# Kernel optimization log

Measured on AMD Instinct MI355X. Metric: run time of the kernel, lower is better.

The kernel has to match this reference:

```python
import jax, jax.numpy as jnp
import numpy as np

N_NODES = 100000
N_EDGES = 1600000
IN_CH = 128
HID = 32
HEADS = 4
OUT_CH = 32
NEG_SLOPE = 0.2  # PyG GATConv default


def _gat_conv(x, src, dst, W, a_src, a_dst, bias, concat):
    """One GATConv layer (eval mode, self-loops already in src/dst).
    x: [N, F_in], W: [F_in, H*C], a_src/a_dst: [H, C], bias: [H*C] or [C].
    """
    N = x.shape[0]
    H, C = a_src.shape
    h = (x @ W).reshape(N, H, C)                      # [N, H, C]
    alpha_s = jnp.einsum('nhc,hc->nh', h, a_src)      # [N, H]
    alpha_d = jnp.einsum('nhc,hc->nh', h, a_dst)      # [N, H]
    logits = jax.nn.leaky_relu(alpha_s[src] + alpha_d[dst], NEG_SLOPE)  # [E, H]
    # segment softmax over incoming edges of each destination node
    m = jax.ops.segment_max(logits, dst, num_segments=N)   # [N, H]
    e = jnp.exp(logits - m[dst])                            # [E, H]
    denom = jax.ops.segment_sum(e, dst, num_segments=N)     # [N, H]
    alpha = e / denom[dst]                                   # [E, H]
    msg = h[src] * alpha[:, :, None]                         # [E, H, C]
    out = jax.ops.segment_sum(msg, dst, num_segments=N)     # [N, H, C]
    out = out.reshape(N, H * C) if concat else out.mean(axis=1)
    return out + bias


def setup_inputs() -> dict:
    key = jax.random.key(0)
    ks = jax.random.split(key, 12)
    x = jax.random.normal(ks[0], (N_NODES, IN_CH), dtype=jnp.float32)
    edge_index = jax.random.randint(ks[1], (2, N_EDGES), 0, N_NODES, dtype=jnp.int64)
    g = 0.1  # glorot-ish scale
    W1 = jax.random.normal(ks[2], (IN_CH, HEADS * HID), dtype=jnp.float32) * g
    a_src1 = jax.random.normal(ks[3], (HEADS, HID), dtype=jnp.float32) * g
    a_dst1 = jax.random.normal(ks[4], (HEADS, HID), dtype=jnp.float32) * g
    b1 = jnp.zeros((HEADS * HID,), dtype=jnp.float32)
    W2 = jax.random.normal(ks[5], (HEADS * HID, OUT_CH), dtype=jnp.float32) * g
    a_src2 = jax.random.normal(ks[6], (1, OUT_CH), dtype=jnp.float32) * g
    a_dst2 = jax.random.normal(ks[7], (1, OUT_CH), dtype=jnp.float32) * g
    b2 = jnp.zeros((OUT_CH,), dtype=jnp.float32)
    return {"x": x, "edge_index": edge_index,
            "W1": W1, "a_src1": a_src1, "a_dst1": a_dst1, "b1": b1,
            "W2": W2, "a_src2": a_src2, "a_dst2": a_dst2, "b2": b2}


def reference(x, edge_index, W1, a_src1, a_dst1, b1, W2, a_src2, a_dst2, b2):
    N = x.shape[0]
    loops = jnp.arange(N, dtype=edge_index.dtype)
    src = jnp.concatenate([edge_index[0], loops])  # add self-loops (PyG default)
    dst = jnp.concatenate([edge_index[1], loops])
    h = _gat_conv(x, src, dst, W1, a_src1, a_dst1, b1, concat=True)   # [N, H*HID]
    h = jax.nn.elu(h)
    out = _gat_conv(h, src, dst, W2, a_src2, a_dst2, b2, concat=False)  # [N, OUT]
    return out
```

## Files before the change

### kernel.cpp

```cpp
#include <hip/hip_runtime.h>
#include <math.h>

#define N_NODES 100000
#define N_EDGES 1600000
#define E_TOT   1700000
#define NEG_SLOPE 0.2f
#define NBUCK 196
#define G1_BLOCKS 1563
#define SCAT_BLOCKS 831
#define PREP_BLOCKS 64

typedef unsigned short ushort_t;
typedef unsigned int uint_t;
typedef __attribute__((ext_vector_type(8))) short bf16x8;
typedef __attribute__((ext_vector_type(4))) float f32x4;

__device__ __forceinline__ float lrelu(float v) { return v > 0.f ? v : NEG_SLOPE * v; }
__device__ __forceinline__ float bf16lo(uint_t u) { return __uint_as_float(u << 16); }
__device__ __forceinline__ float bf16hi(uint_t u) { return __uint_as_float(u & 0xffff0000u); }
__device__ __forceinline__ ushort_t f2bf(float f) {
    uint_t u = __float_as_uint(f);
    u += 0x7fffu + ((u >> 16) & 1u);
    return (ushort_t)(u >> 16);
}

union BU { uint4 u; bf16x8 b; };

__global__ __launch_bounds__(256) void k_prep_hist(const float* __restrict__ W,
                                                   ushort_t* __restrict__ Wb,
                                                   const int* __restrict__ ei,
                                                   int* __restrict__ bucket_cnt)
{
    __shared__ int lbin[NBUCK];
    const int t = threadIdx.x;

    if (blockIdx.x < PREP_BLOCKS) {
        const int idx = blockIdx.x * 256 + t;
        const int j  = idx & 7;
        const int kq = (idx >> 3) & 3;
        const int n  = (idx >> 5) & 15;
        const int tc = (idx >> 9) & 7;
        const int kc = idx >> 12;
        Wb[idx] = f2bf(W[(kc * 32 + kq * 8 + j) * 128 + tc * 16 + n]);
        return;
    }

    const int e0 = (blockIdx.x - PREP_BLOCKS) * 2048 + t;
    for (int i = t; i < NBUCK; i += 256) lbin[i] = 0;
    __syncthreads();
#pragma unroll
    for (int i = 0; i < 8; ++i) {
        const int e = e0 + i * 256;
        if (e < E_TOT) {
            const int d = (e < N_EDGES) ? ei[N_EDGES + e] : (e - N_EDGES);
            atomicAdd(&lbin[d >> 9], 1);
        }
    }
    __syncthreads();
    for (int i = t; i < NBUCK; i += 256)
        if (lbin[i]) atomicAdd(&bucket_cnt[i], lbin[i]);
}

__global__ __launch_bounds__(256) void k_scanB(const int* __restrict__ bucket_cnt,
                                               int* __restrict__ bucket_base,
                                               int* __restrict__ bucket_cursor)
{
    __shared__ int s[256];
    const int t = threadIdx.x;
    const int v = (t < NBUCK) ? bucket_cnt[t] : 0;
    s[t] = v; __syncthreads();
    for (int off = 1; off < 256; off <<= 1) {
        int a = (t >= off) ? s[t - off] : 0;
        __syncthreads();
        s[t] += a;
        __syncthreads();
    }
    const int excl = s[t] - v;
    if (t < NBUCK) {
        bucket_base[t] = excl;
        bucket_cursor[t] = excl;
        if (t == NBUCK - 1) bucket_base[NBUCK] = excl + v;
    }
}

__global__ __launch_bounds__(256) void k_gemm1_scat(const float* __restrict__ x,
                                                    const ushort_t* __restrict__ Wb,
                                                    const float* __restrict__ a_src,
                                                    const float* __restrict__ a_dst,
                                                    ushort_t* __restrict__ hb,
                                                    float* __restrict__ as_,
                                                    float* __restrict__ ad_,
                                                    const int* __restrict__ ei,
                                                    int* __restrict__ bucket_cursor,
                                                    uint2* __restrict__ pairs)
{
    __shared__ int lcnt[NBUCK];
    __shared__ int lbase[NBUCK];
    const int t = threadIdx.x;

    if (blockIdx.x >= G1_BLOCKS) {
        const int e0 = (blockIdx.x - G1_BLOCKS) * 2048 + t;
        for (int i = t; i < NBUCK; i += 256) lcnt[i] = 0;
        __syncthreads();
        int s8[8], d8[8];
#pragma unroll
        for (int i = 0; i < 8; ++i) {
            const int e = e0 + i * 256;
            int s = -1, d = 0;
            if (e < E_TOT) {
                if (e < N_EDGES) { s = ei[e]; d = ei[N_EDGES + e]; }
                else { s = d = e - N_EDGES; }
                atomicAdd(&lcnt[d >> 9], 1);
            }
            s8[i] = s; d8[i] = d;
        }
        __syncthreads();
        for (int i = t; i < NBUCK; i += 256) {
            const int c = lcnt[i];
            lbase[i] = (c > 0) ? atomicAdd(&bucket_cursor[i], c) : 0;
        }
        __syncthreads();
        for (int i = t; i < NBUCK; i += 256) lcnt[i] = 0;
        __syncthreads();
#pragma unroll
        for (int i = 0; i < 8; ++i) {
            if (s8[i] >= 0) {
                const int b = d8[i] >> 9;
                const int pos = lbase[b] + atomicAdd(&lcnt[b], 1);
                pairs[pos] = make_uint2((uint_t)s8[i], (uint_t)d8[i]);
            }
        }
        return;
    }

    const int lane = t & 63;
    const int w = t >> 6;
    const int rbase = blockIdx.x * 64 + w * 16;
    const int li = lane & 15;
    const int g = lane >> 4;

    f32x4 acc[8];
#pragma unroll
    for (int tc = 0; tc < 8; ++tc) acc[tc] = (f32x4){0.f, 0.f, 0.f, 0.f};

    int arow = rbase + li;
    if (arow > N_NODES - 1) arow = N_NODES - 1;
    const float* xr = x + (size_t)arow * 128 + g * 8;

#pragma unroll
    for (int kc = 0; kc < 4; ++kc) {
        const float4 a0 = *(const float4*)(xr + kc * 32);
        const float4 a1 = *(const float4*)(xr + kc * 32 + 4);
        BU au;
        au.u.x = (uint_t)f2bf(a0.x) | ((uint_t)f2bf(a0.y) << 16);
        au.u.y = (uint_t)f2bf(a0.z) | ((uint_t)f2bf(a0.w) << 16);
        au.u.z = (uint_t)f2bf(a1.x) | ((uint_t)f2bf(a1.y) << 16);
        au.u.w = (uint_t)f2bf(a1.z) | ((uint_t)f2bf(a1.w) << 16);
        const bf16x8 af = au.b;
#pragma unroll
        for (int tc = 0; tc < 8; ++tc) {
            const bf16x8 bf = *(const bf16x8*)(Wb + (size_t)(kc * 8 + tc) * 512 + li * 32 + g * 8);
            acc[tc] = __builtin_amdgcn_mfma_f32_16x16x32_bf16(af, bf, acc[tc], 0, 0, 0);
        }
    }

#pragma unroll
    for (int r = 0; r < 4; ++r) {
        const int row = rbase + g * 4 + r;
        if (row < N_NODES) {
            ushort_t* hp = hb + (size_t)row * 128 + li;
#pragma unroll
            for (int tc = 0; tc < 8; ++tc) hp[tc * 16] = f2bf(acc[tc][r]);
        }
    }

    float asv[8], adv[8];
#pragma unroll
    for (int tc = 0; tc < 8; ++tc) {
        asv[tc] = a_src[tc * 16 + li];
        adv[tc] = a_dst[tc * 16 + li];
    }
#pragma unroll
    for (int h = 0; h < 4; ++h) {
#pragma unroll
        for (int r = 0; r < 4; ++r) {
            float ps = acc[2 * h][r] * asv[2 * h] + acc[2 * h + 1][r] * asv[2 * h + 1];
            float pd = acc[2 * h][r] * adv[2 * h] + acc[2 * h + 1][r] * adv[2 * h + 1];
            ps += __shfl_xor(ps, 1); pd += __shfl_xor(pd, 1);
            ps += __shfl_xor(ps, 2); pd += __shfl_xor(pd, 2);
            ps += __shfl_xor(ps, 4); pd += __shfl_xor(pd, 4);
            ps += __shfl_xor(ps, 8); pd += __shfl_xor(pd, 8);
            const int row = rbase + g * 4 + r;
            if (li == 0 && row < N_NODES) {
                as_[row * 4 + h] = ps;
                ad_[row * 4 + h] = pd;
            }
        }
    }
}

__global__ __launch_bounds__(512) void k_buildC(const uint2* __restrict__ pairs,
                                                const int* __restrict__ bucket_base,
                                                int* __restrict__ row_ptr,
                                                int* __restrict__ col_src)
{
    __shared__ int cnt[512];
    __shared__ int cur[512];
    const int b = blockIdx.x, t = threadIdx.x;
    const int bstart = bucket_base[b], bend = bucket_base[b + 1];
    const int node0 = b << 9;

    cnt[t] = 0;
    __syncthreads();
    for (int e = bstart + t; e < bend; e += 512)
        atomicAdd(&cnt[pairs[e].y - node0], 1);
    __syncthreads();

    const int v = cnt[t];
    cur[t] = v; __syncthreads();
    for (int off = 1; off < 512; off <<= 1) {
        int a = (t >= off) ? cur[t - off] : 0;
        __syncthreads();
        cur[t] += a;
        __syncthreads();
    }
    const int excl = bstart + cur[t] - v;
    const int node = node0 + t;
    if (node < N_NODES) row_ptr[node] = excl;
    if (b == 0 && t == 0) row_ptr[N_NODES] = E_TOT;
    cur[t] = excl;
    __syncthreads();

    for (int e = bstart + t; e < bend; e += 512) {
        const uint2 pr = pairs[e];
        const int pos = atomicAdd(&cur[pr.y - node0], 1);
        col_src[pos] = (int)pr.x;
    }
}

__global__ __launch_bounds__(64) void k_agg1(const ushort_t* __restrict__ hb,
                                             const float* __restrict__ as_,
                                             const float* __restrict__ ad_,
                                             const int* __restrict__ row_ptr,
                                             const int* __restrict__ col_src,
                                             const float* __restrict__ bias,
                                             ushort_t* __restrict__ x2b)
{
    __shared__ float sEx[256];
    __shared__ int sSrc[64];
    const int n = blockIdx.x;
    const int lane = threadIdx.x;
    const int start = row_ptr[n], end = row_ptr[n + 1];
    const float4 adv = *(const float4*)(ad_ + (size_t)n * 4);

    const int hsel = lane >> 4;
    const int c0 = lane * 2;
    float2 acc = make_float2(0.f, 0.f);
    float4 ds = make_float4(0.f, 0.f, 0.f, 0.f);
    for (int base = start; base < end; base += 64) {
        const int e = base + lane;
        const int cnt = min(64, end - base);
        float4 ex = make_float4(0.f, 0.f, 0.f, 0.f);
        int s = 0;
        if (e < end) {
            s = col_src[e];
            const float4 av = *(const float4*)(as_ + (size_t)s * 4);
            ex.x = __expf(lrelu(av.x + adv.x));
            ex.y = __expf(lrelu(av.y + adv.y));
            ex.z = __expf(lrelu(av.z + adv.z));
            ex.w = __expf(lrelu(av.w + adv.w));
            ds.x += ex.x; ds.y += ex.y; ds.z += ex.z; ds.w += ex.w;
        }
        __syncthreads();
        *(float4*)(sEx + lane * 4) = ex;
        sSrc[lane] = s;
        __syncthreads();
        for (int i = 0; i < cnt; ++i) {
            const float w = sEx[i * 4 + hsel];
            const uint_t hv = *(const uint_t*)(hb + (size_t)sSrc[i] * 128 + c0);
            acc.x = fmaf(w, bf16lo(hv), acc.x);
            acc.y = fmaf(w, bf16hi(hv), acc.y);
        }
    }
#pragma unroll
    for (int off = 32; off > 0; off >>= 1) {
        ds.x += __shfl_xor(ds.x, off);
        ds.y += __shfl_xor(ds.y, off);
        ds.z += __shfl_xor(ds.z, off);
        ds.w += __shfl_xor(ds.w, off);
    }
    const float denom = hsel == 0 ? ds.x : hsel == 1 ? ds.y : hsel == 2 ? ds.z : ds.w;
    float o0 = acc.x / denom + bias[c0];
    float o1 = acc.y / denom + bias[c0 + 1];
    o0 = o0 > 0.f ? o0 : __expf(o0) - 1.f;
    o1 = o1 > 0.f ? o1 : __expf(o1) - 1.f;
    const uint_t q0 = f2bf(o0), q1 = f2bf(o1);
    *(uint_t*)(x2b + (size_t)n * 128 + c0) = q0 | (q1 << 16);
}

__global__ __launch_bounds__(256) void k_gemm2(const ushort_t* __restrict__ x2b,
                                               const float* __restrict__ W,
                                               const float* __restrict__ a_src,
                                               const float* __restrict__ a_dst,
                                               ushort_t* __restrict__ hb2,
                                               float* __restrict__ as_,
                                               float* __restrict__ ad_)
{
    __shared__ float sW[128 * 32];
    const int t = threadIdx.x;
    {
        const float4* W4 = (const float4*)W;
        float4* s4 = (float4*)sW;
#pragma unroll
        for (int i = 0; i < 4; ++i) s4[t + 256 * i] = W4[t + 256 * i];
    }
    __syncthreads();

    const int rr = t >> 5;
    const int c = t & 31;
    const float a_s = a_src[c], a_d = a_dst[c];

    for (int g = 0; g < 8; ++g) {
        const int row = blockIdx.x * 64 + g * 8 + rr;
        if (row >= N_NODES) continue;
        const ushort_t* xp = x2b + (size_t)row * 128;

        float acc = 0.f;
        for (int k = 0; k < 128; k += 4) {
            const uint2 u = *(const uint2*)(xp + k);
            acc = fmaf(bf16lo(u.x), sW[(k + 0) * 32 + c], acc);
            acc = fmaf(bf16hi(u.x), sW[(k + 1) * 32 + c], acc);
            acc = fmaf(bf16lo(u.y), sW[(k + 2) * 32 + c], acc);
            acc = fmaf(bf16hi(u.y), sW[(k + 3) * 32 + c], acc);
        }

        hb2[(size_t)row * 32 + c] = f2bf(acc);
        float ps = acc * a_s, pd = acc * a_d;
#pragma unroll
        for (int off = 16; off > 0; off >>= 1) {
            ps += __shfl_xor(ps, off);
            pd += __shfl_xor(pd, off);
        }
        if (c == 0) { as_[row] = ps; ad_[row] = pd; }
    }
}

__global__ __launch_bounds__(64) void k_agg2(const ushort_t* __restrict__ hb2,
                                             const float* __restrict__ as_,
                                             const float* __restrict__ ad_,
                                             const int* __restrict__ row_ptr,
                                             const int* __restrict__ col_src,
                                             const float* __restrict__ bias,
                                             float* __restrict__ out)
{
    __shared__ float sEx[64];
    __shared__ int sSrc[64];
    const int n = blockIdx.x;
    const int lane = threadIdx.x;
    const int start = row_ptr[n], end = row_ptr[n + 1];
    const float adn = ad_[n];

    const int quarter = lane >> 4;
    const int cg = lane & 15;
    const int c2 = cg * 2;

    float2 acc = make_float2(0.f, 0.f);
    float dsum = 0.f;
    for (int base = start; base < end; base += 64) {
        const int e = base + lane;
        const int cnt = min(64, end - base);
        float ex = 0.f; int s = 0;
        if (e < end) {
            s = col_src[e];
            ex = __expf(lrelu(as_[s] + adn));
            dsum += ex;
        }
        __syncthreads();
        sEx[lane] = ex;
        sSrc[lane] = s;
        __syncthreads();
        for (int i = quarter; i < cnt; i += 4) {
            const float w = sEx[i];
            const uint_t hv = *(const uint_t*)(hb2 + (size_t)sSrc[i] * 32 + c2);
            acc.x = fmaf(w, bf16lo(hv), acc.x);
            acc.y = fmaf(w, bf16hi(hv), acc.y);
        }
    }
#pragma unroll
    for (int off = 32; off > 0; off >>= 1) dsum += __shfl_xor(dsum, off);
    acc.x += __shfl_xor(acc.x, 16);
    acc.y += __shfl_xor(acc.y, 16);
    acc.x += __shfl_xor(acc.x, 32);
    acc.y += __shfl_xor(acc.y, 32);
    if (quarter == 0) {
        float2 o = make_float2(acc.x / dsum + bias[c2], acc.y / dsum + bias[c2 + 1]);
        *(float2*)(out + (size_t)n * 32 + c2) = o;
    }
}

extern "C" void kernel_launch(void* const* d_in, const int* in_sizes, int n_in,
                              void* d_out, int out_size, void* d_ws, size_t ws_size,
                              hipStream_t stream)
{
    const float* x      = (const float*)d_in[0];
    const int*   ei     = (const int*)d_in[1];
    const float* W1     = (const float*)d_in[2];
    const float* a_src1 = (const float*)d_in[3];
    const float* a_dst1 = (const float*)d_in[4];
    const float* b1     = (const float*)d_in[5];
    const float* W2     = (const float*)d_in[6];
    const float* a_src2 = (const float*)d_in[7];
    const float* a_dst2 = (const float*)d_in[8];
    const float* b2     = (const float*)d_in[9];
    float* out = (float*)d_out;

    char* p = (char*)d_ws;
    auto alloc = [&](size_t bytes) { char* q = p; p += (bytes + 255) & ~(size_t)255; return q; };
    ushort_t* h1b = (ushort_t*)alloc((size_t)N_NODES * 128 * 2);
    ushort_t* x2b = (ushort_t*)alloc((size_t)N_NODES * 128 * 2);
    ushort_t* h2b = (ushort_t*)alloc((size_t)N_NODES * 32 * 2);
    ushort_t* Wb  = (ushort_t*)alloc((size_t)16384 * 2);
    float* as1    = (float*)alloc((size_t)N_NODES * 4 * 4);
    float* ad1    = (float*)alloc((size_t)N_NODES * 4 * 4);
    float* as2    = (float*)alloc((size_t)N_NODES * 4);
    float* ad2    = (float*)alloc((size_t)N_NODES * 4);
    int* row_ptr  = (int*)alloc((size_t)(N_NODES + 1) * 4);
    int* bucket_cnt    = (int*)alloc((NBUCK + 1) * 4);
    int* bucket_base   = (int*)alloc((NBUCK + 1) * 4);
    int* bucket_cursor = (int*)alloc((NBUCK + 1) * 4);
    uint2* pairs  = (uint2*)alloc((size_t)E_TOT * 8);
    int* col_src  = (int*)alloc((size_t)E_TOT * 4);

    (void)hipMemsetAsync(bucket_cnt, 0, (NBUCK + 1) * 4, stream);

    k_prep_hist<<<PREP_BLOCKS + SCAT_BLOCKS, 256, 0, stream>>>(W1, Wb, ei, bucket_cnt);
    k_scanB<<<1, 256, 0, stream>>>(bucket_cnt, bucket_base, bucket_cursor);
    k_gemm1_scat<<<G1_BLOCKS + SCAT_BLOCKS, 256, 0, stream>>>(
        x, Wb, a_src1, a_dst1, h1b, as1, ad1, ei, bucket_cursor, pairs);
    k_buildC<<<NBUCK, 512, 0, stream>>>(pairs, bucket_base, row_ptr, col_src);
    k_agg1<<<N_NODES, 64, 0, stream>>>(h1b, as1, ad1, row_ptr, col_src, b1, x2b);
    k_gemm2<<<(N_NODES + 63) / 64, 256, 0, stream>>>(x2b, W2, a_src2, a_dst2, h2b, as2, ad2);
    k_agg2<<<N_NODES, 64, 0, stream>>>(h2b, as2, ad2, row_ptr, col_src, b2, out);
}
```

Before: 250.3 us.

## Fuse layer-2 projection into layer-1 aggregation and coarsen edge scatter blocks

The second-layer GEMM (128->32 projection plus attention coefficient dots) is folded into the end of k_agg1. Each node's ELU output is staged in shared memory and multiplied by a transposed bf16 copy of W2 that is prepared in the prep kernel. This removes the x2b intermediate write and re-read and one kernel launch. Separately, the histogram and scatter blocks now each process a larger contiguous chunk of edges with fewer blocks, so there are fewer global atomics on bucket counters. The cost is more serial work per block and more per-node compute in agg1. Edge indices are also re-read in the scatter's second pass instead of being kept in registers.

```diff
diff --git a/kernel.cpp b/kernel.cpp
--- a/kernel.cpp
+++ b/kernel.cpp
@@ -7,8 +7,9 @@
 #define NEG_SLOPE 0.2f
 #define NBUCK 196
 #define G1_BLOCKS 1563
-#define SCAT_BLOCKS 831
-#define PREP_BLOCKS 64
+#define SCAT2 256
+#define ECHUNK 6641
+#define PREP_BLOCKS 80
 
 typedef unsigned short ushort_t;
 typedef unsigned int uint_t;
@@ -26,8 +27,10 @@
 
 union BU { uint4 u; bf16x8 b; };
 
-__global__ __launch_bounds__(256) void k_prep_hist(const float* __restrict__ W,
+__global__ __launch_bounds__(256) void k_prep_hist(const float* __restrict__ W1,
+                                                   const float* __restrict__ W2,
                                                    ushort_t* __restrict__ Wb,
+                                                   ushort_t* __restrict__ Wc2,
                                                    const int* __restrict__ ei,
                                                    int* __restrict__ bucket_cnt)
 {
@@ -36,25 +39,29 @@
 
     if (blockIdx.x < PREP_BLOCKS) {
         const int idx = blockIdx.x * 256 + t;
-        const int j  = idx & 7;
-        const int kq = (idx >> 3) & 3;
-        const int n  = (idx >> 5) & 15;
-        const int tc = (idx >> 9) & 7;
-        const int kc = idx >> 12;
-        Wb[idx] = f2bf(W[(kc * 32 + kq * 8 + j) * 128 + tc * 16 + n]);
+        if (idx < 16384) {
+            const int j  = idx & 7;
+            const int kq = (idx >> 3) & 3;
+            const int n  = (idx >> 5) & 15;
+            const int tc = (idx >> 9) & 7;
+            const int kc = idx >> 12;
+            Wb[idx] = f2bf(W1[(kc * 32 + kq * 8 + j) * 128 + tc * 16 + n]);
+        } else {
+            const int i2 = idx - 16384;
+            const int c = i2 >> 7, k = i2 & 127;
+            Wc2[i2] = f2bf(W2[k * 32 + c]);
+        }
         return;
     }
 
-    const int e0 = (blockIdx.x - PREP_BLOCKS) * 2048 + t;
+    const int eb = blockIdx.x - PREP_BLOCKS;
+    const int estart = eb * ECHUNK;
+    const int eend = min(estart + ECHUNK, E_TOT);
     for (int i = t; i < NBUCK; i += 256) lbin[i] = 0;
     __syncthreads();
-#pragma unroll
-    for (int i = 0; i < 8; ++i) {
-        const int e = e0 + i * 256;
-        if (e < E_TOT) {
-            const int d = (e < N_EDGES) ? ei[N_EDGES + e] : (e - N_EDGES);
-            atomicAdd(&lbin[d >> 9], 1);
-        }
+    for (int e = estart + t; e < eend; e += 256) {
+        const int d = (e < N_EDGES) ? ei[N_EDGES + e] : (e - N_EDGES);
+        atomicAdd(&lbin[d >> 9], 1);
     }
     __syncthreads();
     for (int i = t; i < NBUCK; i += 256)
@@ -99,20 +106,14 @@
     const int t = threadIdx.x;
 
     if (blockIdx.x >= G1_BLOCKS) {
-        const int e0 = (blockIdx.x - G1_BLOCKS) * 2048 + t;
+        const int eb = blockIdx.x - G1_BLOCKS;
+        const int estart = eb * ECHUNK;
+        const int eend = min(estart + ECHUNK, E_TOT);
         for (int i = t; i < NBUCK; i += 256) lcnt[i] = 0;
         __syncthreads();
-        int s8[8], d8[8];
-#pragma unroll
-        for (int i = 0; i < 8; ++i) {
-            const int e = e0 + i * 256;
-            int s = -1, d = 0;
-            if (e < E_TOT) {
-                if (e < N_EDGES) { s = ei[e]; d = ei[N_EDGES + e]; }
-                else { s = d = e - N_EDGES; }
-                atomicAdd(&lcnt[d >> 9], 1);
-            }
-            s8[i] = s; d8[i] = d;
+        for (int e = estart + t; e < eend; e += 256) {
+            const int d = (e < N_EDGES) ? ei[N_EDGES + e] : (e - N_EDGES);
+            atomicAdd(&lcnt[d >> 9], 1);
         }
         __syncthreads();
         for (int i = t; i < NBUCK; i += 256) {
@@ -122,13 +123,13 @@
         __syncthreads();
         for (int i = t; i < NBUCK; i += 256) lcnt[i] = 0;
         __syncthreads();
-#pragma unroll
-        for (int i = 0; i < 8; ++i) {
-            if (s8[i] >= 0) {
-                const int b = d8[i] >> 9;
-                const int pos = lbase[b] + atomicAdd(&lcnt[b], 1);
-                pairs[pos] = make_uint2((uint_t)s8[i], (uint_t)d8[i]);
-            }
+        for (int e = estart + t; e < eend; e += 256) {
+            int s, d;
+            if (e < N_EDGES) { s = ei[e]; d = ei[N_EDGES + e]; }
+            else { s = d = e - N_EDGES; }
+            const int b = d >> 9;
+            const int pos = lbase[b] + atomicAdd(&lcnt[b], 1);
+            pairs[pos] = make_uint2((uint_t)s, (uint_t)d);
         }
         return;
     }
@@ -244,10 +245,16 @@
                                              const int* __restrict__ row_ptr,
                                              const int* __restrict__ col_src,
                                              const float* __restrict__ bias,
-                                             ushort_t* __restrict__ x2b)
+                                             const ushort_t* __restrict__ Wc2,
+                                             const float* __restrict__ a_src2,
+                                             const float* __restrict__ a_dst2,
+                                             ushort_t* __restrict__ h2b,
+                                             float* __restrict__ as2,
+                                             float* __restrict__ ad2)
 {
     __shared__ float sEx[256];
     __shared__ int sSrc[64];
+    __shared__ float sX[128];
     const int n = blockIdx.x;
     const int lane = threadIdx.x;
     const int start = row_ptr[n], end = row_ptr[n + 1];
@@ -294,55 +301,30 @@
     float o1 = acc.y / denom + bias[c0 + 1];
     o0 = o0 > 0.f ? o0 : __expf(o0) - 1.f;
     o1 = o1 > 0.f ? o1 : __expf(o1) - 1.f;
-    const uint_t q0 = f2bf(o0), q1 = f2bf(o1);
-    *(uint_t*)(x2b + (size_t)n * 128 + c0) = q0 | (q1 << 16);
-}
-
-__global__ __launch_bounds__(256) void k_gemm2(const ushort_t* __restrict__ x2b,
-                                               const float* __restrict__ W,
-                                               const float* __restrict__ a_src,
-                                               const float* __restrict__ a_dst,
-                                               ushort_t* __restrict__ hb2,
-                                               float* __restrict__ as_,
-                                               float* __restrict__ ad_)
-{
-    __shared__ float sW[128 * 32];
-    const int t = threadIdx.x;
-    {
-        const float4* W4 = (const float4*)W;
-        float4* s4 = (float4*)sW;
-#pragma unroll
-        for (int i = 0; i < 4; ++i) s4[t + 256 * i] = W4[t + 256 * i];
-    }
-    __syncthreads();
-
-    const int rr = t >> 5;
-    const int c = t & 31;
-    const float a_s = a_src[c], a_d = a_dst[c];
-
-    for (int g = 0; g < 8; ++g) {
-        const int row = blockIdx.x * 64 + g * 8 + rr;
-        if (row >= N_NODES) continue;
-        const ushort_t* xp = x2b + (size_t)row * 128;
-
-        float acc = 0.f;
-        for (int k = 0; k < 128; k += 4) {
-            const uint2 u = *(const uint2*)(xp + k);
-            acc = fmaf(bf16lo(u.x), sW[(k + 0) * 32 + c], acc);
-            acc = fmaf(bf16hi(u.x), sW[(k + 1) * 32 + c], acc);
-            acc = fmaf(bf16lo(u.y), sW[(k + 2) * 32 + c], acc);
-            acc = fmaf(bf16hi(u.y), sW[(k + 3) * 32 + c], acc);
-        }
-
-        hb2[(size_t)row * 32 + c] = f2bf(acc);
-        float ps = acc * a_s, pd = acc * a_d;
-#pragma unroll
-        for (int off = 16; off > 0; off >>= 1) {
-            ps += __shfl_xor(ps, off);
-            pd += __shfl_xor(pd, off);
-        }
-        if (c == 0) { as_[row] = ps; ad_[row] = pd; }
-    }
+
+    sX[c0] = o0; sX[c0 + 1] = o1;
+    __syncthreads();
+    const int c = lane & 31, hf = lane >> 5;
+    const ushort_t* wc = Wc2 + c * 128 + hf * 64;
+    const float* xk = sX + hf * 64;
+    float h2 = 0.f;
+#pragma unroll
+    for (int k = 0; k < 64; k += 4) {
+        const uint2 u = *(const uint2*)(wc + k);
+        h2 = fmaf(xk[k + 0], bf16lo(u.x), h2);
+        h2 = fmaf(xk[k + 1], bf16hi(u.x), h2);
+        h2 = fmaf(xk[k + 2], bf16lo(u.y), h2);
+        h2 = fmaf(xk[k + 3], bf16hi(u.y), h2);
+    }
+    h2 += __shfl_xor(h2, 32);
+    float ps = h2 * a_src2[c], pd = h2 * a_dst2[c];
+#pragma unroll
+    for (int off = 16; off > 0; off >>= 1) {
+        ps += __shfl_xor(ps, off);
+        pd += __shfl_xor(pd, off);
+    }
+    if (lane == 0) { as2[n] = ps; ad2[n] = pd; }
+    if (hf == 0) h2b[(size_t)n * 32 + c] = f2bf(h2);
 }
 
 __global__ __launch_bounds__(64) void k_agg2(const ushort_t* __restrict__ hb2,
@@ -417,9 +399,9 @@
     char* p = (char*)d_ws;
     auto alloc = [&](size_t bytes) { char* q = p; p += (bytes + 255) & ~(size_t)255; return q; };
     ushort_t* h1b = (ushort_t*)alloc((size_t)N_NODES * 128 * 2);
-    ushort_t* x2b = (ushort_t*)alloc((size_t)N_NODES * 128 * 2);
     ushort_t* h2b = (ushort_t*)alloc((size_t)N_NODES * 32 * 2);
     ushort_t* Wb  = (ushort_t*)alloc((size_t)16384 * 2);
+    ushort_t* Wc2 = (ushort_t*)alloc((size_t)4096 * 2);
     float* as1    = (float*)alloc((size_t)N_NODES * 4 * 4);
     float* ad1    = (float*)alloc((size_t)N_NODES * 4 * 4);
     float* as2    = (float*)alloc((size_t)N_NODES * 4);
@@ -433,12 +415,12 @@
 
     (void)hipMemsetAsync(bucket_cnt, 0, (NBUCK + 1) * 4, stream);
 
-    k_prep_hist<<<PREP_BLOCKS + SCAT_BLOCKS, 256, 0, stream>>>(W1, Wb, ei, bucket_cnt);
+    k_prep_hist<<<PREP_BLOCKS + SCAT2, 256, 0, stream>>>(W1, W2, Wb, Wc2, ei, bucket_cnt);
     k_scanB<<<1, 256, 0, stream>>>(bucket_cnt, bucket_base, bucket_cursor);
-    k_gemm1_scat<<<G1_BLOCKS + SCAT_BLOCKS, 256, 0, stream>>>(
+    k_gemm1_scat<<<G1_BLOCKS + SCAT2, 256, 0, stream>>>(
         x, Wb, a_src1, a_dst1, h1b, as1, ad1, ei, bucket_cursor, pairs);
     k_buildC<<<NBUCK, 512, 0, stream>>>(pairs, bucket_base, row_ptr, col_src);
-    k_agg1<<<N_NODES, 64, 0, stream>>>(h1b, as1, ad1, row_ptr, col_src, b1, x2b);
-    k_gemm2<<<(N_NODES + 63) / 64, 256, 0, stream>>>(x2b, W2, a_src2, a_dst2, h2b, as2, ad2);
+    k_agg1<<<N_NODES, 64, 0, stream>>>(h1b, as1, ad1, row_ptr, col_src, b1,
+                                       Wc2, a_src2, a_dst2, h2b, as2, ad2);
     k_agg2<<<N_NODES, 64, 0, stream>>>(h2b, as2, ad2, row_ptr, col_src, b2, out);
 }
```

Result: slower. 256.2 us (+2.3%).
